# Optimization experiments

Hardware: AMD Instinct MI355X
Metric: run time of the kernel (lower is better)

The kernel has to match this reference:

```python
import jax, jax.numpy as jnp
import numpy as np

BN_EPS = 1e-5


def setup_inputs() -> dict:
    key = jax.random.key(0)
    ks = jax.random.split(key, 4)
    S, B, F, P, T, H, W = 4, 2, 64, 16, 32, 64, 64
    HID = 32
    feats = jax.random.normal(ks[0], (S, B, F, T, H, W), dtype=jnp.float32)
    p_s = jax.random.normal(ks[1], (B, P, T, H, W), dtype=jnp.float32)
    w1 = jax.random.normal(ks[2], (HID, F + P), dtype=jnp.float32) * (1.0 / np.sqrt(F + P))
    w2 = jax.random.normal(ks[3], (HID,), dtype=jnp.float32) * (1.0 / np.sqrt(HID))
    return {
        "feats": feats,
        "p_s": p_s,
        "w1": w1,
        "bn_gamma": jnp.ones((HID,), jnp.float32),
        "bn_beta": jnp.zeros((HID,), jnp.float32),
        "bn_mean": jnp.zeros((HID,), jnp.float32),
        "bn_var": jnp.ones((HID,), jnp.float32),
        "w2": w2,
        "b2": jnp.zeros((1,), jnp.float32),
    }


def reference(feats, p_s, w1, bn_gamma, bn_beta, bn_mean, bn_var, w2, b2):
    # feats: [S,B,F,T,H,W]; p_s: [B,P,T,H,W]
    F = feats.shape[2]
    w1_f, w1_p = w1[:, :F], w1[:, F:]
    # 1x1x1 conv on concat([f, p_s]) == split contraction; avoids materializing concat
    h = jnp.einsum('of,sbfthw->sbothw', w1_f, feats) \
        + jnp.einsum('op,bpthw->bothw', w1_p, p_s)[None]
    # BatchNorm3d (inference form) folded to scale/shift, then ReLU
    scale = bn_gamma / jnp.sqrt(bn_var + BN_EPS)
    shift = bn_beta - bn_mean * scale
    h = jax.nn.relu(h * scale[:, None, None, None] + shift[:, None, None, None])
    # second 1x1x1 conv: hidden -> 1 logit per branch
    logits = jnp.einsum('sbothw,o->sbthw', h, w2) + b2[0]
    alpha = jax.nn.softmax(logits, axis=0)            # softmax over branches S
    out = jnp.einsum('sbfthw,sbthw->bfthw', feats, alpha)
    return out, jnp.moveaxis(alpha, 0, 1)             # out:[B,F,T,H,W], alpha:[B,S,T,H,W]
```

## Files before the change

kernel.cpp:

```cpp
#include <hip/hip_runtime.h>
#include <hip/hip_bf16.h>
#include <stdint.h>

#define THW   131072
#define NS    4
#define NB    2
#define NF    64
#define NP    16
#define HID   32
#define BN_EPS 1e-5f

typedef short  bf16x8  __attribute__((ext_vector_type(8)));
typedef float  f32x16  __attribute__((ext_vector_type(16)));

union FragU { uint32_t u[4]; bf16x8 v; uint4 q; };

__device__ __forceinline__ uint32_t pk2(float a, float b) {
    __hip_bfloat162 h = __float22bfloat162_rn(make_float2(a, b));
    uint32_t r;
    __builtin_memcpy(&r, &h, sizeof(r));
    return r;
}
__device__ __forceinline__ float lo16(uint32_t u) { return __builtin_bit_cast(float, u << 16); }
__device__ __forceinline__ float hi16(uint32_t u) { return __builtin_bit_cast(float, u & 0xFFFF0000u); }

__global__ __launch_bounds__(256, 2) void gssm_kernel(
    const float* __restrict__ feats, const float* __restrict__ ps,
    const float* __restrict__ w1,    const float* __restrict__ gamma,
    const float* __restrict__ beta,  const float* __restrict__ mean,
    const float* __restrict__ var,   const float* __restrict__ w2,
    float* __restrict__ out)
{
    __shared__ __align__(16) uint32_t w1lds[32 * 44];
    __shared__ float2 tbl[HID];

    const int tid = threadIdx.x;
    for (int t = tid; t < 1280; t += 256) {
        float2 v = ((const float2*)w1)[t];
        int o = t / 40, cp = t - o * 40;
        float sc = gamma[o] * rsqrtf(var[o] + BN_EPS);
        w1lds[o * 44 + (cp >> 3) * 8 + (cp & 7)] = pk2(v.x * sc, v.y * sc);
    }
    if (tid < HID) {
        float sc = gamma[tid] * rsqrtf(var[tid] + BN_EPS);
        tbl[tid] = make_float2(beta[tid] - mean[tid] * sc, w2[tid]);
    }
    __syncthreads();

    const int lane = tid & 63;
    const int wv   = tid >> 6;
    const int hi   = lane >> 5;
    const int ln   = lane & 31;

    const int tile = blockIdx.x * 4 + wv;
    const int pix0 = tile * 32;
    const int b    = pix0 >> 17;
    const int thw  = (pix0 & (THW - 1)) + ln;

    FragU afr[5];
    {
        const uint32_t abase = (uint32_t)(ln * 44 + hi * 4);
        #pragma unroll
        for (int k = 0; k < 5; ++k)
            afr[k].q = *((const uint4*)&w1lds[abase + k * 8]);
    }

    FragU bp;
    {
        const float* pb = ps + ((long)(b * NP + hi * 8)) * THW + thw;
        float pv[8];
        #pragma unroll
        for (int r = 0; r < 8; ++r) pv[r] = pb[(long)r * THW];
        #pragma unroll
        for (int r = 0; r < 4; ++r) bp.u[r] = pk2(pv[2 * r], pv[2 * r + 1]);
    }

    const float* fbase = feats + ((long)(b * NF + hi * 8)) * THW + thw;
    const long   sstr  = (long)NB * NF * THW;

    auto issue = [&](int s, float* fv) {
        const float* fb = fbase + (long)s * sstr;
        #pragma unroll
        for (int k = 0; k < 4; ++k)
            #pragma unroll
            for (int j = 0; j < 8; ++j)
                fv[k * 8 + j] = fb[(long)(k * 16 + j) * THW];
    };
    auto pack = [&](FragU* pk, const float* fv) {
        #pragma unroll
        for (int k = 0; k < 4; ++k)
            #pragma unroll
            for (int r = 0; r < 4; ++r)
                pk[k].u[r] = pk2(fv[k * 8 + 2 * r], fv[k * 8 + 2 * r + 1]);
    };
    auto logit = [&](const FragU* pk) -> float {
        f32x16 acc;
        #pragma unroll
        for (int r = 0; r < 16; ++r) acc[r] = 0.f;
        acc = __builtin_amdgcn_mfma_f32_32x32x16_bf16(afr[4].v, bp.v,    acc, 0, 0, 0);
        acc = __builtin_amdgcn_mfma_f32_32x32x16_bf16(afr[0].v, pk[0].v, acc, 0, 0, 0);
        acc = __builtin_amdgcn_mfma_f32_32x32x16_bf16(afr[1].v, pk[1].v, acc, 0, 0, 0);
        acc = __builtin_amdgcn_mfma_f32_32x32x16_bf16(afr[2].v, pk[2].v, acc, 0, 0, 0);
        acc = __builtin_amdgcn_mfma_f32_32x32x16_bf16(afr[3].v, pk[3].v, acc, 0, 0, 0);
        float pp[4] = {0.f, 0.f, 0.f, 0.f};
        #pragma unroll
        for (int r = 0; r < 16; ++r) {
            float2 t = tbl[(r & 3) + 8 * (r >> 2) + 4 * hi];
            float h = fmaxf(acc[r] + t.x, 0.f);
            pp[r & 3] = fmaf(h, t.y, pp[r & 3]);
        }
        float part = (pp[0] + pp[1]) + (pp[2] + pp[3]);
        return part + __shfl_xor(part, 32);
    };

    float fvA[32], fvB[32];
    FragU pk0[4], pk1[4], pk2f[4], pk3[4];
    float lg0, lg1, lg2, lg3;

    issue(0, fvA);
    pack(pk0, fvA);
    issue(1, fvB);
    lg0 = logit(pk0);
    pack(pk1, fvB);
    issue(2, fvA);
    lg1 = logit(pk1);
    pack(pk2f, fvA);
    issue(3, fvB);
    lg2 = logit(pk2f);
    pack(pk3, fvB);
    lg3 = logit(pk3);

    const float m   = fmaxf(fmaxf(lg0, lg1), fmaxf(lg2, lg3));
    const float e0  = __expf(lg0 - m), e1 = __expf(lg1 - m);
    const float e2  = __expf(lg2 - m), e3 = __expf(lg3 - m);
    const float inv = 1.f / (e0 + e1 + e2 + e3);
    const float a0 = e0 * inv, a1 = e1 * inv, a2 = e2 * inv, a3 = e3 * inv;

    float* ob = out + ((long)(b * NF + hi * 8)) * THW + thw;
    #pragma unroll
    for (int k = 0; k < 4; ++k)
        #pragma unroll
        for (int r = 0; r < 4; ++r) {
            float vlo = a0 * lo16(pk0[k].u[r]);
            float vhi = a0 * hi16(pk0[k].u[r]);
            vlo = fmaf(a1, lo16(pk1[k].u[r]), vlo);
            vhi = fmaf(a1, hi16(pk1[k].u[r]), vhi);
            vlo = fmaf(a2, lo16(pk2f[k].u[r]), vlo);
            vhi = fmaf(a2, hi16(pk2f[k].u[r]), vhi);
            vlo = fmaf(a3, lo16(pk3[k].u[r]), vlo);
            vhi = fmaf(a3, hi16(pk3[k].u[r]), vhi);
            ob[(long)(k * 16 + 2 * r)     * THW] = vlo;
            ob[(long)(k * 16 + 2 * r + 1) * THW] = vhi;
        }

    float* ab = out + (long)NB * NF * THW + ((long)(b * NS + hi * 2)) * THW + thw;
    ab[0]   = hi ? a2 : a0;
    ab[THW] = hi ? a3 : a1;
}

extern "C" void kernel_launch(void* const* d_in, const int* in_sizes, int n_in,
                              void* d_out, int out_size, void* d_ws, size_t ws_size,
                              hipStream_t stream) {
    const float* feats = (const float*)d_in[0];
    const float* ps    = (const float*)d_in[1];
    const float* w1    = (const float*)d_in[2];
    const float* gamma = (const float*)d_in[3];
    const float* beta  = (const float*)d_in[4];
    const float* mean  = (const float*)d_in[5];
    const float* var   = (const float*)d_in[6];
    const float* w2    = (const float*)d_in[7];
    float* out = (float*)d_out;

    dim3 grid(2048), block(256);
    hipLaunchKernelGGL(gssm_kernel, grid, block, 0, stream,
                       feats, ps, w1, gamma, beta, mean, var, w2, out);
}
```

Before: 93.99 us.

## Stage feats and p_s through LDS via async global_load_lds double buffering

New measurement: 95.96 us. 1.02x slower.

```diff
diff --git a/kernel.cpp b/kernel.cpp
--- a/kernel.cpp
+++ b/kernel.cpp
@@ -9,6 +9,7 @@
 #define NP    16
 #define HID   32
 #define BN_EPS 1e-5f
+#define PXT   128
 
 typedef short  bf16x8  __attribute__((ext_vector_type(8)));
 typedef float  f32x16  __attribute__((ext_vector_type(16)));
@@ -23,6 +24,12 @@
 }
 __device__ __forceinline__ float lo16(uint32_t u) { return __builtin_bit_cast(float, u << 16); }
 __device__ __forceinline__ float hi16(uint32_t u) { return __builtin_bit_cast(float, u & 0xFFFF0000u); }
+
+__device__ __forceinline__ void glds16(const float* g, void* l) {
+    __builtin_amdgcn_global_load_lds(
+        (const __attribute__((address_space(1))) uint32_t*)g,
+        (__attribute__((address_space(3))) uint32_t*)l, 16, 0, 0);
+}
 
 __global__ __launch_bounds__(256, 2) void gssm_kernel(
     const float* __restrict__ feats, const float* __restrict__ ps,
@@ -31,10 +38,17 @@
     const float* __restrict__ var,   const float* __restrict__ w2,
     float* __restrict__ out)
 {
+    __shared__ __align__(16) float    fbuf[2][NF][PXT];
+    __shared__ __align__(16) float    pbuf[NP][PXT];
     __shared__ __align__(16) uint32_t w1lds[32 * 44];
     __shared__ float2 tbl[HID];
 
-    const int tid = threadIdx.x;
+    const int tid  = threadIdx.x;
+    const int lane = tid & 63;
+    const int wv   = tid >> 6;
+    const int hi   = lane >> 5;
+    const int ln   = lane & 31;
+
     for (int t = tid; t < 1280; t += 256) {
         float2 v = ((const float2*)w1)[t];
         int o = t / 40, cp = t - o * 40;
@@ -45,17 +59,37 @@
         float sc = gamma[tid] * rsqrtf(var[tid] + BN_EPS);
         tbl[tid] = make_float2(beta[tid] - mean[tid] * sc, w2[tid]);
     }
-    __syncthreads();
-
-    const int lane = tid & 63;
-    const int wv   = tid >> 6;
-    const int hi   = lane >> 5;
-    const int ln   = lane & 31;
-
-    const int tile = blockIdx.x * 4 + wv;
-    const int pix0 = tile * 32;
-    const int b    = pix0 >> 17;
-    const int thw  = (pix0 & (THW - 1)) + ln;
+
+    const int px0g = blockIdx.x * PXT;
+    const int b    = px0g >> 17;
+    const int px0  = px0g & (THW - 1);
+
+    const float* featsb = feats + (long)b * NF * THW + px0;
+    const float* psb    = ps    + (long)b * NP * THW + px0;
+    const long   sstr   = (long)NB * NF * THW;
+
+    const long pl_off = (long)(lane >> 5) * THW + (ln << 2);
+    const int  f0     = wv * 16;
+
+    auto stage_feats = [&](int s, int buf) {
+        const float* base = featsb + (long)s * sstr;
+        #pragma unroll
+        for (int i = 0; i < 8; ++i) {
+            int f = f0 + i * 2;
+            glds16(base + (long)f * THW + pl_off, (void*)&fbuf[buf][f][0]);
+        }
+    };
+
+    {
+        #pragma unroll
+        for (int i = 0; i < 2; ++i) {
+            int p = wv * 4 + i * 2;
+            glds16(psb + (long)p * THW + pl_off, (void*)&pbuf[p][0]);
+        }
+    }
+    stage_feats(0, 0);
+    asm volatile("s_waitcnt vmcnt(0) lgkmcnt(0)" ::: "memory");
+    __builtin_amdgcn_s_barrier();
 
     FragU afr[5];
     {
@@ -64,36 +98,28 @@
         for (int k = 0; k < 5; ++k)
             afr[k].q = *((const uint4*)&w1lds[abase + k * 8]);
     }
+    float sh[16], wo[16];
+    #pragma unroll
+    for (int r = 0; r < 16; ++r) {
+        float2 t = tbl[(r & 3) + 8 * (r >> 2) + 4 * hi];
+        sh[r] = t.x;
+        wo[r] = t.y;
+    }
+
+    const int pxloc = wv * 32 + ln;
 
     FragU bp;
-    {
-        const float* pb = ps + ((long)(b * NP + hi * 8)) * THW + thw;
-        float pv[8];
-        #pragma unroll
-        for (int r = 0; r < 8; ++r) pv[r] = pb[(long)r * THW];
-        #pragma unroll
-        for (int r = 0; r < 4; ++r) bp.u[r] = pk2(pv[2 * r], pv[2 * r + 1]);
-    }
-
-    const float* fbase = feats + ((long)(b * NF + hi * 8)) * THW + thw;
-    const long   sstr  = (long)NB * NF * THW;
-
-    auto issue = [&](int s, float* fv) {
-        const float* fb = fbase + (long)s * sstr;
-        #pragma unroll
-        for (int k = 0; k < 4; ++k)
-            #pragma unroll
-            for (int j = 0; j < 8; ++j)
-                fv[k * 8 + j] = fb[(long)(k * 16 + j) * THW];
-    };
-    auto pack = [&](FragU* pk, const float* fv) {
-        #pragma unroll
-        for (int k = 0; k < 4; ++k)
+    #pragma unroll
+    for (int r = 0; r < 4; ++r)
+        bp.u[r] = pk2(pbuf[hi * 8 + 2 * r][pxloc], pbuf[hi * 8 + 2 * r + 1][pxloc]);
+
+    auto consume = [&](int buf, FragU* pk) -> float {
+        #pragma unroll
+        for (int kb = 0; kb < 4; ++kb)
             #pragma unroll
             for (int r = 0; r < 4; ++r)
-                pk[k].u[r] = pk2(fv[k * 8 + 2 * r], fv[k * 8 + 2 * r + 1]);
-    };
-    auto logit = [&](const FragU* pk) -> float {
+                pk[kb].u[r] = pk2(fbuf[buf][kb * 16 + hi * 8 + 2 * r][pxloc],
+                                  fbuf[buf][kb * 16 + hi * 8 + 2 * r + 1][pxloc]);
         f32x16 acc;
         #pragma unroll
         for (int r = 0; r < 16; ++r) acc[r] = 0.f;
@@ -105,36 +131,40 @@
         float pp[4] = {0.f, 0.f, 0.f, 0.f};
         #pragma unroll
         for (int r = 0; r < 16; ++r) {
-            float2 t = tbl[(r & 3) + 8 * (r >> 2) + 4 * hi];
-            float h = fmaxf(acc[r] + t.x, 0.f);
-            pp[r & 3] = fmaf(h, t.y, pp[r & 3]);
+            float h = fmaxf(acc[r] + sh[r], 0.f);
+            pp[r & 3] = fmaf(h, wo[r], pp[r & 3]);
         }
         float part = (pp[0] + pp[1]) + (pp[2] + pp[3]);
         return part + __shfl_xor(part, 32);
     };
 
-    float fvA[32], fvB[32];
     FragU pk0[4], pk1[4], pk2f[4], pk3[4];
     float lg0, lg1, lg2, lg3;
 
-    issue(0, fvA);
-    pack(pk0, fvA);
-    issue(1, fvB);
-    lg0 = logit(pk0);
-    pack(pk1, fvB);
-    issue(2, fvA);
-    lg1 = logit(pk1);
-    pack(pk2f, fvA);
-    issue(3, fvB);
-    lg2 = logit(pk2f);
-    pack(pk3, fvB);
-    lg3 = logit(pk3);
+    stage_feats(1, 1);
+    lg0 = consume(0, pk0);
+    asm volatile("s_waitcnt vmcnt(0)" ::: "memory");
+    __builtin_amdgcn_s_barrier();
+
+    stage_feats(2, 0);
+    lg1 = consume(1, pk1);
+    asm volatile("s_waitcnt vmcnt(0)" ::: "memory");
+    __builtin_amdgcn_s_barrier();
+
+    stage_feats(3, 1);
+    lg2 = consume(0, pk2f);
+    asm volatile("s_waitcnt vmcnt(0)" ::: "memory");
+    __builtin_amdgcn_s_barrier();
+
+    lg3 = consume(1, pk3);
 
     const float m   = fmaxf(fmaxf(lg0, lg1), fmaxf(lg2, lg3));
     const float e0  = __expf(lg0 - m), e1 = __expf(lg1 - m);
     const float e2  = __expf(lg2 - m), e3 = __expf(lg3 - m);
     const float inv = 1.f / (e0 + e1 + e2 + e3);
     const float a0 = e0 * inv, a1 = e1 * inv, a2 = e2 * inv, a3 = e3 * inv;
+
+    const int thw = px0 + pxloc;
 
     float* ob = out + ((long)(b * NF + hi * 8)) * THW + thw;
     #pragma unroll
```
